# Performance work log

Hardware: AMD Instinct MI355X
Metric: run time of the kernel (lower is better)

The kernel has to match this reference:

```python
import jax, jax.numpy as jnp
import numpy as np

N = 100000
E = 1600000
F_IN = 32
H = 64
O = 64
L = 4
EPS = 1e-5


def setup_inputs() -> dict:
    key = jax.random.key(0)
    ks = jax.random.split(key, 16)
    x = jax.random.normal(ks[0], (N, F_IN), dtype=jnp.float32)
    edge_index = jax.random.randint(ks[1], (2, E), 0, N, dtype=jnp.int64)

    def xavier(k, shape):
        fan_in, fan_out = shape[-2], shape[-1]
        lim = (6.0 / (fan_in + fan_out)) ** 0.5
        return jax.random.uniform(k, shape, jnp.float32, -lim, lim)

    return {
        "x": x,
        "edge_index": edge_index,
        "W_embed": xavier(ks[2], (F_IN, H)),
        "b_embed": jnp.zeros((H,), jnp.float32),
        "conv_W": xavier(ks[3], (L, H, H)),
        "conv_b": jnp.zeros((L, H), jnp.float32),
        "bn_gamma": jnp.ones((L, H), jnp.float32),
        "bn_beta": jnp.zeros((L, H), jnp.float32),
        "W_out": xavier(ks[4], (H, O)),
        "b_out": jnp.zeros((O,), jnp.float32),
    }


def reference(x, edge_index, W_embed, b_embed, conv_W, conv_b, bn_gamma, bn_beta, W_out, b_out):
    src, dst = edge_index[0], edge_index[1]
    # GCN symmetric normalization with self-loops: deg counts incoming edges + 1
    deg = jax.ops.segment_sum(jnp.ones((E,), x.dtype), dst, num_segments=N) + 1.0
    dinv = deg ** -0.5                      # [N]
    norm_e = dinv[src] * dinv[dst]          # [E]
    self_norm = dinv * dinv                 # [N]  (self-loop weight)

    h = x @ W_embed + b_embed               # node embedding [N, H]

    for i in range(L):
        xw = h @ conv_W[i]                  # linear transform first (PyG GCNConv)
        msg = xw[src] * norm_e[:, None]     # gather + edge scaling [E, H]
        agg = jax.ops.segment_sum(msg, dst, num_segments=N)
        h = agg + xw * self_norm[:, None] + conv_b[i]
        # BatchNorm1d (training-mode batch stats, biased variance)
        mu = jnp.mean(h, axis=0)
        var = jnp.mean((h - mu) ** 2, axis=0)
        h = bn_gamma[i] * (h - mu) * jax.lax.rsqrt(var + EPS) + bn_beta[i]
        h = jax.nn.relu(h)
        # dropout is identity in inference

    pooled = jnp.mean(h, axis=0, keepdims=True)   # [1, H]
    return pooled @ W_out + b_out                 # [1, O]
```

## Files before the change

### kernel.cpp

```cpp
#include <hip/hip_runtime.h>

#define N_NODES 100000
#define N_EDGES 1600000
#define F_IN    32
#define HD      64
#define EPS     1e-5f
#define SCAN_B  512
#define SCAN_G  ((N_NODES + SCAN_B - 1) / SCAN_B)
#define NSHADOW 64
#define NP      196
#define PWS     9
#define NB1     250
#define EPB     6400

typedef __attribute__((ext_vector_type(8))) short short8v;
typedef __attribute__((ext_vector_type(4))) float f32x4;
typedef __attribute__((ext_vector_type(2))) float f32x2;

__device__ __forceinline__ unsigned bf16r(float f) {
    unsigned u = __float_as_uint(f);
    return (u + 0x7fffu + ((u >> 16) & 1u)) >> 16;
}
__device__ __forceinline__ unsigned pack2(float lo, float hi) {
    return bf16r(lo) | (bf16r(hi) << 16);
}
__device__ __forceinline__ float unlo(unsigned u) { return __uint_as_float(u << 16); }
__device__ __forceinline__ float unhi(unsigned u) { return __uint_as_float(u & 0xffff0000u); }

__device__ __forceinline__ unsigned pack_fp8x4(float a, float b, float c, float d) {
    int v = __builtin_amdgcn_cvt_pk_fp8_f32(a, b, 0, false);
    v = __builtin_amdgcn_cvt_pk_fp8_f32(c, d, v, true);
    return (unsigned)v;
}

__global__ void k_detect(const int* __restrict__ ei, int* __restrict__ flag) {
    if (threadIdx.x == 0 && blockIdx.x == 0) {
        int all_zero = 1;
        for (int k = 0; k < 64; ++k)
            if (ei[2 * k + 1] != 0) { all_zero = 0; break; }
        *flag = all_zero;
    }
}

__device__ __forceinline__ int load_src(const int* ei, int e, int is64) {
    return is64 ? ei[2 * e] : ei[e];
}
__device__ __forceinline__ int load_dst(const int* ei, int e, int is64) {
    return is64 ? ei[2 * (N_EDGES + e)] : ei[N_EDGES + e];
}

__global__ void __launch_bounds__(256)
k_p1_hist(const int* __restrict__ ei, const int* __restrict__ flag, int* __restrict__ hcnt) {
    __shared__ int hist[NP];
    int t = threadIdx.x, b = blockIdx.x;
    if (t < NP) hist[t] = 0;
    __syncthreads();
    int is64 = *flag;
#pragma unroll 5
    for (int i = 0; i < 25; ++i) {
        int e = b * EPB + i * 256 + t;
        int d = load_dst(ei, e, is64);
        atomicAdd(&hist[d >> PWS], 1);
    }
    __syncthreads();
    if (t < NP) hcnt[t * NB1 + b] = hist[t];
}

__global__ void k_p2scan(const int* __restrict__ hcnt, int* __restrict__ off_bp,
                         int* __restrict__ ptotal) {
    __shared__ int ls[256];
    int t = threadIdx.x, p = blockIdx.x;
    int v = (t < NB1) ? hcnt[p * NB1 + t] : 0;
    ls[t] = v;
    __syncthreads();
    for (int off = 1; off < 256; off <<= 1) {
        int u = (t >= off) ? ls[t - off] : 0;
        __syncthreads();
        ls[t] += u;
        __syncthreads();
    }
    if (t < NB1) off_bp[p * NB1 + t] = ls[t] - v;
    if (t == 255) ptotal[p] = ls[255];
}

__global__ void k_p3scan(const int* __restrict__ ptotal, int* __restrict__ pbase) {
    __shared__ int ls[256];
    int t = threadIdx.x;
    int v = (t < NP) ? ptotal[t] : 0;
    ls[t] = v;
    __syncthreads();
    for (int off = 1; off < 256; off <<= 1) {
        int u = (t >= off) ? ls[t - off] : 0;
        __syncthreads();
        ls[t] += u;
        __syncthreads();
    }
    if (t < NP) pbase[t] = ls[t] - v;
}

__global__ void __launch_bounds__(256)
k_p2_scatter(const int* __restrict__ ei, const int* __restrict__ flag,
             const int* __restrict__ off_bp, const int* __restrict__ pbase,
             uint2* __restrict__ part_buf) {
    __shared__ int cursor[NP];
    int t = threadIdx.x, b = blockIdx.x;
    if (t < NP) cursor[t] = pbase[t] + off_bp[t * NB1 + b];
    __syncthreads();
    int is64 = *flag;
#pragma unroll 5
    for (int i = 0; i < 25; ++i) {
        int e = b * EPB + i * 256 + t;
        int s = load_src(ei, e, is64);
        int d = load_dst(ei, e, is64);
        int slot = atomicAdd(&cursor[d >> PWS], 1);
        part_buf[slot] = make_uint2((unsigned)s, (unsigned)d);
    }
}

__global__ void __launch_bounds__(256)
k_p3a_deg(const uint2* __restrict__ part_buf, const int* __restrict__ pbase,
          const int* __restrict__ ptotal, int* __restrict__ deg,
          float* __restrict__ dinv) {
    __shared__ int hist[512];
    int t = threadIdx.x, p = blockIdx.x;
    hist[t] = 0; hist[t + 256] = 0;
    __syncthreads();
    int beg = pbase[p], cnt = ptotal[p];
    for (int r = t; r < cnt; r += 256)
        atomicAdd(&hist[part_buf[beg + r].y & 511], 1);
    __syncthreads();
    int n0 = (p << PWS) + t;
    if (n0 < N_NODES) {
        deg[n0] = hist[t];
        dinv[n0] = rsqrtf((float)hist[t] + 1.0f);
    }
    if (n0 + 256 < N_NODES) {
        deg[n0 + 256] = hist[t + 256];
        dinv[n0 + 256] = rsqrtf((float)hist[t + 256] + 1.0f);
    }
}

__global__ void __launch_bounds__(256)
k_p3b_csr(const uint2* __restrict__ part_buf, const int* __restrict__ pbase,
          const int* __restrict__ ptotal, const int* __restrict__ row_start,
          int* __restrict__ csr_src) {
    __shared__ int cur[512];
    int t = threadIdx.x, p = blockIdx.x;
    int n0 = (p << PWS) + t;
    cur[t]       = (n0 < N_NODES)       ? row_start[n0]       : 0;
    cur[t + 256] = (n0 + 256 < N_NODES) ? row_start[n0 + 256] : 0;
    __syncthreads();
    int beg = pbase[p], cnt = ptotal[p];
    for (int r = t; r < cnt; r += 256) {
        uint2 rec = part_buf[beg + r];
        int slot = atomicAdd(&cur[rec.y & 511], 1);
        csr_src[slot] = (int)rec.x;
    }
}

__global__ void k_scan1(const int* __restrict__ deg, int* __restrict__ bsum) {
    int t = threadIdx.x;
    int i = blockIdx.x * SCAN_B + t;
    __shared__ int ls[SCAN_B];
    ls[t] = (i < N_NODES) ? deg[i] : 0;
    __syncthreads();
    for (int off = SCAN_B / 2; off > 0; off >>= 1) {
        if (t < off) ls[t] += ls[t + off];
        __syncthreads();
    }
    if (t == 0) bsum[blockIdx.x] = ls[0];
}

__global__ void k_scan2(const int* __restrict__ bsum, int* __restrict__ boff,
                        int* __restrict__ row_start_last) {
    __shared__ int ls[256];
    int t = threadIdx.x;
    ls[t] = (t < SCAN_G) ? bsum[t] : 0;
    __syncthreads();
    for (int off = 1; off < 256; off <<= 1) {
        int u = (t >= off) ? ls[t - off] : 0;
        __syncthreads();
        ls[t] += u;
        __syncthreads();
    }
    boff[t] = (t == 0) ? 0 : ls[t - 1];
    if (t == 255) *row_start_last = ls[255];
}

__global__ void k_scan3(const int* __restrict__ deg, const int* __restrict__ boff,
                        int* __restrict__ row_start) {
    int t = threadIdx.x;
    int i = blockIdx.x * SCAN_B + t;
    int v = (i < N_NODES) ? deg[i] : 0;
    __shared__ int ls[SCAN_B];
    ls[t] = v;
    __syncthreads();
    for (int off = 1; off < SCAN_B; off <<= 1) {
        int u = (t >= off) ? ls[t - off] : 0;
        __syncthreads();
        ls[t] += u;
        __syncthreads();
    }
    if (i < N_NODES) row_start[i] = boff[blockIdx.x] + ls[t] - v;
}

__global__ void k_embed(const float* __restrict__ x, const float* __restrict__ W,
                        const float* __restrict__ b, unsigned* __restrict__ hb) {
    __shared__ float Ws[F_IN * HD];
    __shared__ float xs[4 * F_IN];
    int t = threadIdx.x;
    for (int i = t; i < F_IN * HD; i += 256) Ws[i] = W[i];
    if (t < 4 * F_IN) {
        int r = t >> 5, c = t & 31;
        int node = blockIdx.x * 4 + r;
        xs[t] = (node < N_NODES) ? x[node * F_IN + c] : 0.f;
    }
    __syncthreads();
    int r = t >> 6, j = t & 63;
    int node = blockIdx.x * 4 + r;
    float acc = b[j];
#pragma unroll
    for (int k = 0; k < F_IN; ++k)
        acc = fmaf(xs[r * F_IN + k], Ws[k * HD + j], acc);
    float other = __shfl_xor(acc, 1);
    if (node < N_NODES && (j & 1) == 0)
        hb[node * 32 + (j >> 1)] = pack2(acc, other);
}

__global__ void __launch_bounds__(256)
k_gemm_mfma(const unsigned* __restrict__ Ab, const float* __restrict__ W,
            const float* __restrict__ coef, const float* __restrict__ dinv,
            unsigned* __restrict__ Cf8) {
    __shared__ short Wt[64 * 72];
    __shared__ float Cs[4][16 * 66];
    int t = threadIdx.x;

    for (int i = t; i < HD * HD; i += 256) {
        int k = i >> 6, j = i & 63;
        Wt[j * 72 + k] = (short)bf16r(W[i]);
    }
    __syncthreads();

    int wid = t >> 6, lane = t & 63;
    int rlane = lane & 15, kb = lane >> 4;
    int base = blockIdx.x * 64 + wid * 16;
    int arow = base + rlane;
    if (arow > N_NODES - 1) arow = N_NODES - 1;
    bool has_coef = (coef != nullptr);

    short8v afrag[2];
#pragma unroll
    for (int h = 0; h < 2; ++h) {
        uint4 p = *reinterpret_cast<const uint4*>(Ab + arow * 32 + h * 16 + kb * 4);
        union { uint4 u; short8v s; } cv;
        if (has_coef) {
            int k0 = h * 32 + kb * 8;
            float v0 = unlo(p.x), v1 = unhi(p.x), v2 = unlo(p.y), v3 = unhi(p.y);
            float v4 = unlo(p.z), v5 = unhi(p.z), v6 = unlo(p.w), v7 = unhi(p.w);
            v0 = fmaxf(fmaf(coef[k0 + 0], v0, coef[64 + k0 + 0]), 0.f);
            v1 = fmaxf(fmaf(coef[k0 + 1], v1, coef[64 + k0 + 1]), 0.f);
            v2 = fmaxf(fmaf(coef[k0 + 2], v2, coef[64 + k0 + 2]), 0.f);
            v3 = fmaxf(fmaf(coef[k0 + 3], v3, coef[64 + k0 + 3]), 0.f);
            v4 = fmaxf(fmaf(coef[k0 + 4], v4, coef[64 + k0 + 4]), 0.f);
            v5 = fmaxf(fmaf(coef[k0 + 5], v5, coef[64 + k0 + 5]), 0.f);
            v6 = fmaxf(fmaf(coef[k0 + 6], v6, coef[64 + k0 + 6]), 0.f);
            v7 = fmaxf(fmaf(coef[k0 + 7], v7, coef[64 + k0 + 7]), 0.f);
            cv.u.x = pack2(v0, v1); cv.u.y = pack2(v2, v3);
            cv.u.z = pack2(v4, v5); cv.u.w = pack2(v6, v7);
        } else {
            cv.u = p;
        }
        afrag[h] = cv.s;
    }

    f32x4 acc[4];
#pragma unroll
    for (int nt = 0; nt < 4; ++nt) acc[nt] = (f32x4){0.f, 0.f, 0.f, 0.f};

#pragma unroll
    for (int nt = 0; nt < 4; ++nt) {
        int col = nt * 16 + rlane;
#pragma unroll
        for (int h = 0; h < 2; ++h) {
            short8v b = *reinterpret_cast<const short8v*>(&Wt[col * 72 + h * 32 + kb * 8]);
            acc[nt] = __builtin_amdgcn_mfma_f32_16x16x32_bf16(afrag[h], b, acc[nt], 0, 0, 0);
        }
    }

    float dv[4];
#pragma unroll
    for (int r = 0; r < 4; ++r) {
        int g = base + kb * 4 + r;
        dv[r] = dinv[g > N_NODES - 1 ? N_NODES - 1 : g];
    }
#pragma unroll
    for (int nt = 0; nt < 4; ++nt) {
        int col = nt * 16 + rlane;
#pragma unroll
        for (int r = 0; r < 4; ++r)
            Cs[wid][(kb * 4 + r) * 66 + col] = acc[nt][r] * dv[r];
    }
    __syncthreads();

#pragma unroll
    for (int u = 0; u < 4; ++u) {
        int o = u * 64 + lane;
        int row = o >> 4, q = o & 15;
        int node = blockIdx.x * 64 + wid * 16 + row;
        if (node < N_NODES) {
            const float* cp = &Cs[wid][row * 66 + q * 4];
            Cf8[node * 16 + q] = pack_fp8x4(cp[0], cp[1], cp[2], cp[3]);
        }
    }
}

__global__ void __launch_bounds__(256)
k_gather_stats(const unsigned* __restrict__ xwf8, const int* __restrict__ row_start,
               const int* __restrict__ csr_src, const float* __restrict__ dinv,
               const float* __restrict__ cb, uint2* __restrict__ hb2,
               float* __restrict__ stats_sh) {
    int t = threadIdx.x;
    int q = t & 15;
    int r = t >> 4;
    float cb0 = cb[q * 4 + 0], cb1 = cb[q * 4 + 1];
    float cb2 = cb[q * 4 + 2], cb3 = cb[q * 4 + 3];
    float4 st_s = {0.f, 0.f, 0.f, 0.f}, st_q = {0.f, 0.f, 0.f, 0.f};

#pragma unroll
    for (int i = 0; i < 4; ++i) {
        int n = blockIdx.x * 64 + r * 4 + i;
        bool valid = (n < N_NODES);
        int beg = 0, end = 0;
        if (valid) { beg = row_start[n]; end = row_start[n + 1]; }
        float4 a0 = {0.f,0.f,0.f,0.f}, a1 = {0.f,0.f,0.f,0.f};
        float4 a2 = {0.f,0.f,0.f,0.f}, a3 = {0.f,0.f,0.f,0.f};
        if (valid) {
            unsigned p = xwf8[n * 16 + q];
            f32x2 lo = __builtin_amdgcn_cvt_pk_f32_fp8((int)p, false);
            f32x2 hi = __builtin_amdgcn_cvt_pk_f32_fp8((int)p, true);
            a0.x = lo[0]; a0.y = lo[1]; a0.z = hi[0]; a0.w = hi[1];
        }
        int e = beg;
        for (; e + 3 < end; e += 4) {
            int s0 = csr_src[e],     s1 = csr_src[e + 1];
            int s2 = csr_src[e + 2], s3 = csr_src[e + 3];
            unsigned p0 = xwf8[s0 * 16 + q], p1 = xwf8[s1 * 16 + q];
            unsigned p2 = xwf8[s2 * 16 + q], p3 = xwf8[s3 * 16 + q];
            f32x2 l0 = __builtin_amdgcn_cvt_pk_f32_fp8((int)p0, false);
            f32x2 h0 = __builtin_amdgcn_cvt_pk_f32_fp8((int)p0, true);
            f32x2 l1 = __builtin_amdgcn_cvt_pk_f32_fp8((int)p1, false);
            f32x2 h1 = __builtin_amdgcn_cvt_pk_f32_fp8((int)p1, true);
            f32x2 l2 = __builtin_amdgcn_cvt_pk_f32_fp8((int)p2, false);
            f32x2 h2 = __builtin_amdgcn_cvt_pk_f32_fp8((int)p2, true);
            f32x2 l3 = __builtin_amdgcn_cvt_pk_f32_fp8((int)p3, false);
            f32x2 h3 = __builtin_amdgcn_cvt_pk_f32_fp8((int)p3, true);
            a0.x += l0[0]; a0.y += l0[1]; a0.z += h0[0]; a0.w += h0[1];
            a1.x += l1[0]; a1.y += l1[1]; a1.z += h1[0]; a1.w += h1[1];
            a2.x += l2[0]; a2.y += l2[1]; a2.z += h2[0]; a2.w += h2[1];
            a3.x += l3[0]; a3.y += l3[1]; a3.z += h3[0]; a3.w += h3[1];
        }
        for (; e < end; ++e) {
            int s0 = csr_src[e];
            unsigned p0 = xwf8[s0 * 16 + q];
            f32x2 l0 = __builtin_amdgcn_cvt_pk_f32_fp8((int)p0, false);
            f32x2 h0 = __builtin_amdgcn_cvt_pk_f32_fp8((int)p0, true);
            a0.x += l0[0]; a0.y += l0[1]; a0.z += h0[0]; a0.w += h0[1];
        }
        float dn = valid ? dinv[n] : 0.f;
        float4 h;
        h.x = fmaf(a0.x + a1.x + a2.x + a3.x, dn, cb0);
        h.y = fmaf(a0.y + a1.y + a2.y + a3.y, dn, cb1);
        h.z = fmaf(a0.z + a1.z + a2.z + a3.z, dn, cb2);
        h.w = fmaf(a0.w + a1.w + a2.w + a3.w, dn, cb3);
        if (valid) {
            uint2 o;
            o.x = pack2(h.x, h.y);
            o.y = pack2(h.z, h.w);
            hb2[n * 16 + q] = o;
            st_s.x += h.x; st_s.y += h.y; st_s.z += h.z; st_s.w += h.w;
            st_q.x = fmaf(h.x, h.x, st_q.x); st_q.y = fmaf(h.y, h.y, st_q.y);
            st_q.z = fmaf(h.z, h.z, st_q.z); st_q.w = fmaf(h.w, h.w, st_q.w);
        }
    }

    __shared__ float4 ls_s[256], ls_q[256];
    ls_s[t] = st_s; ls_q[t] = st_q;
    __syncthreads();
    if (t < 16) {
        float4 ss = ls_s[t], qq = ls_q[t];
        for (int rr = 1; rr < 16; ++rr) {
            float4 u = ls_s[rr * 16 + t], v = ls_q[rr * 16 + t];
            ss.x += u.x; ss.y += u.y; ss.z += u.z; ss.w += u.w;
            qq.x += v.x; qq.y += v.y; qq.z += v.z; qq.w += v.w;
        }
        float* sh = stats_sh + (blockIdx.x & (NSHADOW - 1)) * 128;
        atomicAdd(&sh[4 * t + 0], ss.x);
        atomicAdd(&sh[4 * t + 1], ss.y);
        atomicAdd(&sh[4 * t + 2], ss.z);
        atomicAdd(&sh[4 * t + 3], ss.w);
        atomicAdd(&sh[64 + 4 * t + 0], qq.x);
        atomicAdd(&sh[64 + 4 * t + 1], qq.y);
        atomicAdd(&sh[64 + 4 * t + 2], qq.z);
        atomicAdd(&sh[64 + 4 * t + 3], qq.w);
    }
}

__global__ void k_bn_coef(const float* __restrict__ stats_sh, const float* __restrict__ gamma,
                          const float* __restrict__ beta, float* __restrict__ coef) {
    int j = threadIdx.x;
    float s = 0.f, s2 = 0.f;
    for (int c = 0; c < NSHADOW; ++c) {
        s  += stats_sh[c * 128 + j];
        s2 += stats_sh[c * 128 + 64 + j];
    }
    float mu  = s * (1.0f / N_NODES);
    float var = s2 * (1.0f / N_NODES) - mu * mu;
    float rs  = rsqrtf(var + EPS);
    float a   = gamma[j] * rs;
    coef[j]      = a;
    coef[64 + j] = fmaf(-a, mu, beta[j]);
}

__global__ void k_pool(const unsigned* __restrict__ hb, const float* __restrict__ coef,
                       float* __restrict__ pooled) {
    int t = threadIdx.x;
    int j = t & 63, rg = t >> 6;
    float a = coef[j], c = coef[64 + j];
    float s = 0.f;
    for (int n = blockIdx.x * 4 + rg; n < N_NODES; n += gridDim.x * 4) {
        unsigned p = hb[n * 32 + (j >> 1)];
        float v = (j & 1) ? unhi(p) : unlo(p);
        s += fmaxf(fmaf(a, v, c), 0.f);
    }
    __shared__ float ls[256];
    ls[t] = s;
    __syncthreads();
    if (t < 64)
        atomicAdd(&pooled[j], ls[t] + ls[t + 64] + ls[t + 128] + ls[t + 192]);
}

__global__ void k_out(const float* __restrict__ pooled, const float* __restrict__ Wout,
                      const float* __restrict__ bout, float* __restrict__ out) {
    int o = threadIdx.x;
    float acc = bout[o];
#pragma unroll
    for (int k = 0; k < HD; ++k)
        acc = fmaf(pooled[k] * (1.0f / N_NODES), Wout[k * HD + o], acc);
    out[o] = acc;
}

extern "C" void kernel_launch(void* const* d_in, const int* in_sizes, int n_in,
                              void* d_out, int out_size, void* d_ws, size_t ws_size,
                              hipStream_t stream) {
    const float* x        = (const float*)d_in[0];
    const int*   ei       = (const int*)  d_in[1];
    const float* W_embed  = (const float*)d_in[2];
    const float* b_embed  = (const float*)d_in[3];
    const float* conv_W   = (const float*)d_in[4];
    const float* conv_b   = (const float*)d_in[5];
    const float* bn_gamma = (const float*)d_in[6];
    const float* bn_beta  = (const float*)d_in[7];
    const float* W_out    = (const float*)d_in[8];
    const float* b_out    = (const float*)d_in[9];
    float* out = (float*)d_out;

    float* ws = (float*)d_ws;
    int*   deg       = (int*)ws;
    float* dinv      = ws + N_NODES;
    int*   row_start = (int*)(ws + 2 * N_NODES);
    float* small     = ws + 3 * N_NODES + 8;
    int*   bsum      = (int*)small;
    int*   boff      = (int*)(small + 256);
    float* stats_sh  = small + 512;
    float* pooled    = small + 8704;
    float* coef      = small + 8768;
    int*   flag      = (int*)(small + 9280);
    int*   csr_src   = (int*)(small + 9344);
    int*   hcnt      = (int*)(small + 9344 + N_EDGES);
    int*   off_bp    = hcnt + NP * NB1;
    int*   ptotal    = off_bp + NP * NB1;
    int*   pbase     = ptotal + 256;
    uint2* part_buf  = (uint2*)(pbase + 256);
    float* bufA      = (float*)(part_buf + N_EDGES);
    float* bufB      = bufA + N_NODES * 32;

    k_detect<<<1, 64, 0, stream>>>(ei, flag);
    k_p1_hist<<<NB1, 256, 0, stream>>>(ei, flag, hcnt);
    k_p2scan<<<NP, 256, 0, stream>>>(hcnt, off_bp, ptotal);
    k_p3scan<<<1, 256, 0, stream>>>(ptotal, pbase);
    k_p2_scatter<<<NB1, 256, 0, stream>>>(ei, flag, off_bp, pbase, part_buf);
    k_p3a_deg<<<NP, 256, 0, stream>>>(part_buf, pbase, ptotal, deg, dinv);
    k_scan1<<<SCAN_G, SCAN_B, 0, stream>>>(deg, bsum);
    k_scan2<<<1, 256, 0, stream>>>(bsum, boff, ((int*)(ws + 2 * N_NODES)) + N_NODES);
    k_scan3<<<SCAN_G, SCAN_B, 0, stream>>>(deg, boff, row_start);
    k_embed<<<(N_NODES + 3) / 4, 256, 0, stream>>>(x, W_embed, b_embed, (unsigned*)bufA);
    k_p3b_csr<<<NP, 256, 0, stream>>>(part_buf, pbase, ptotal, row_start, csr_src);

    for (int l = 0; l < 4; ++l) {
        k_gemm_mfma<<<(N_NODES + 63) / 64, 256, 0, stream>>>(
            (const unsigned*)bufA, conv_W + l * HD * HD,
            l ? coef + (l - 1) * 128 : nullptr, dinv, (unsigned*)bufB);
        hipMemsetAsync(stats_sh, 0, NSHADOW * 128 * sizeof(float), stream);
        k_gather_stats<<<(N_NODES + 63) / 64, 256, 0, stream>>>(
            (const unsigned*)bufB, row_start, csr_src, dinv, conv_b + l * HD,
            (uint2*)bufA, stats_sh);
        k_bn_coef<<<1, 64, 0, stream>>>(stats_sh, bn_gamma + l * HD, bn_beta + l * HD,
                                        coef + l * 128);
    }

    hipMemsetAsync(pooled, 0, 64 * sizeof(float), stream);
    k_pool<<<1024, 256, 0, stream>>>((const unsigned*)bufA, coef + 3 * 128, pooled);
    k_out<<<1, 64, 0, stream>>>(pooled, W_out, b_out, out);
}
```

Before: 348.2 us.

## Split gather into two feature-half planes and fuse CSR build with scan

The GEMM now writes its fp8 output as two separate 32-feature planes, and the gather kernel runs twice per layer, once per plane. Each pass touches a 3.2MB working set, which makes random row gathers more likely to hit in cache, at the cost of reading the CSR indices twice. The degree count, prefix scan and CSR fill are merged into one per-partition kernel with a local block scan, removing four launches and the deg array. Stats buffers for all layers are cleared by one memset up front instead of one per layer.

```diff
diff --git a/kernel.cpp b/kernel.cpp
--- a/kernel.cpp
+++ b/kernel.cpp
@@ -5,13 +5,12 @@
 #define F_IN    32
 #define HD      64
 #define EPS     1e-5f
-#define SCAN_B  512
-#define SCAN_G  ((N_NODES + SCAN_B - 1) / SCAN_B)
 #define NSHADOW 64
 #define NP      196
 #define PWS     9
 #define NB1     250
 #define EPB     6400
+#define NPLANE  (N_NODES * 8)
 
 typedef __attribute__((ext_vector_type(8))) short short8v;
 typedef __attribute__((ext_vector_type(4))) float f32x4;
@@ -118,10 +117,12 @@
 }
 
 __global__ void __launch_bounds__(256)
-k_p3a_deg(const uint2* __restrict__ part_buf, const int* __restrict__ pbase,
-          const int* __restrict__ ptotal, int* __restrict__ deg,
-          float* __restrict__ dinv) {
+k_p3_build(const uint2* __restrict__ part_buf, const int* __restrict__ pbase,
+           const int* __restrict__ ptotal, int* __restrict__ row_start,
+           float* __restrict__ dinv, int* __restrict__ csr_src) {
     __shared__ int hist[512];
+    __shared__ int s2[256];
+    __shared__ int cur[512];
     int t = threadIdx.x, p = blockIdx.x;
     hist[t] = 0; hist[t + 256] = 0;
     __syncthreads();
@@ -129,79 +130,28 @@
     for (int r = t; r < cnt; r += 256)
         atomicAdd(&hist[part_buf[beg + r].y & 511], 1);
     __syncthreads();
-    int n0 = (p << PWS) + t;
-    if (n0 < N_NODES) {
-        deg[n0] = hist[t];
-        dinv[n0] = rsqrtf((float)hist[t] + 1.0f);
-    }
-    if (n0 + 256 < N_NODES) {
-        deg[n0 + 256] = hist[t + 256];
-        dinv[n0 + 256] = rsqrtf((float)hist[t + 256] + 1.0f);
-    }
-}
-
-__global__ void __launch_bounds__(256)
-k_p3b_csr(const uint2* __restrict__ part_buf, const int* __restrict__ pbase,
-          const int* __restrict__ ptotal, const int* __restrict__ row_start,
-          int* __restrict__ csr_src) {
-    __shared__ int cur[512];
-    int t = threadIdx.x, p = blockIdx.x;
-    int n0 = (p << PWS) + t;
-    cur[t]       = (n0 < N_NODES)       ? row_start[n0]       : 0;
-    cur[t + 256] = (n0 + 256 < N_NODES) ? row_start[n0 + 256] : 0;
-    __syncthreads();
-    int beg = pbase[p], cnt = ptotal[p];
+    int d0 = hist[2 * t], d1 = hist[2 * t + 1];
+    s2[t] = d0 + d1;
+    __syncthreads();
+    for (int off = 1; off < 256; off <<= 1) {
+        int u = (t >= off) ? s2[t - off] : 0;
+        __syncthreads();
+        s2[t] += u;
+        __syncthreads();
+    }
+    int ex = (t == 0) ? 0 : s2[t - 1];
+    int rs0 = beg + ex, rs1 = beg + ex + d0;
+    int n0 = (p << PWS) + 2 * t;
+    if (n0 < N_NODES)     { row_start[n0]     = rs0; dinv[n0]     = rsqrtf((float)d0 + 1.f); }
+    if (n0 + 1 < N_NODES) { row_start[n0 + 1] = rs1; dinv[n0 + 1] = rsqrtf((float)d1 + 1.f); }
+    cur[2 * t] = rs0; cur[2 * t + 1] = rs1;
+    if (p == NP - 1 && t == 0) row_start[N_NODES] = N_EDGES;
+    __syncthreads();
     for (int r = t; r < cnt; r += 256) {
         uint2 rec = part_buf[beg + r];
         int slot = atomicAdd(&cur[rec.y & 511], 1);
         csr_src[slot] = (int)rec.x;
     }
-}
-
-__global__ void k_scan1(const int* __restrict__ deg, int* __restrict__ bsum) {
-    int t = threadIdx.x;
-    int i = blockIdx.x * SCAN_B + t;
-    __shared__ int ls[SCAN_B];
-    ls[t] = (i < N_NODES) ? deg[i] : 0;
-    __syncthreads();
-    for (int off = SCAN_B / 2; off > 0; off >>= 1) {
-        if (t < off) ls[t] += ls[t + off];
-        __syncthreads();
-    }
-    if (t == 0) bsum[blockIdx.x] = ls[0];
-}
-
-__global__ void k_scan2(const int* __restrict__ bsum, int* __restrict__ boff,
-                        int* __restrict__ row_start_last) {
-    __shared__ int ls[256];
-    int t = threadIdx.x;
-    ls[t] = (t < SCAN_G) ? bsum[t] : 0;
-    __syncthreads();
-    for (int off = 1; off < 256; off <<= 1) {
-        int u = (t >= off) ? ls[t - off] : 0;
-        __syncthreads();
-        ls[t] += u;
-        __syncthreads();
-    }
-    boff[t] = (t == 0) ? 0 : ls[t - 1];
-    if (t == 255) *row_start_last = ls[255];
-}
-
-__global__ void k_scan3(const int* __restrict__ deg, const int* __restrict__ boff,
-                        int* __restrict__ row_start) {
-    int t = threadIdx.x;
-    int i = blockIdx.x * SCAN_B + t;
-    int v = (i < N_NODES) ? deg[i] : 0;
-    __shared__ int ls[SCAN_B];
-    ls[t] = v;
-    __syncthreads();
-    for (int off = 1; off < SCAN_B; off <<= 1) {
-        int u = (t >= off) ? ls[t - off] : 0;
-        __syncthreads();
-        ls[t] += u;
-        __syncthreads();
-    }
-    if (i < N_NODES) row_start[i] = boff[blockIdx.x] + ls[t] - v;
 }
 
 __global__ void k_embed(const float* __restrict__ x, const float* __restrict__ W,
@@ -309,33 +259,35 @@
         int node = blockIdx.x * 64 + wid * 16 + row;
         if (node < N_NODES) {
             const float* cp = &Cs[wid][row * 66 + q * 4];
-            Cf8[node * 16 + q] = pack_fp8x4(cp[0], cp[1], cp[2], cp[3]);
+            unsigned val = pack_fp8x4(cp[0], cp[1], cp[2], cp[3]);
+            if (q < 8) Cf8[node * 8 + q] = val;
+            else       Cf8[NPLANE + node * 8 + (q - 8)] = val;
         }
     }
 }
 
 __global__ void __launch_bounds__(256)
-k_gather_stats(const unsigned* __restrict__ xwf8, const int* __restrict__ row_start,
+k_gather_stats(const unsigned* __restrict__ plane, const int* __restrict__ row_start,
                const int* __restrict__ csr_src, const float* __restrict__ dinv,
-               const float* __restrict__ cb, uint2* __restrict__ hb2,
-               float* __restrict__ stats_sh) {
+               const float* __restrict__ cb ,
+               uint2* __restrict__ hb2, float* __restrict__ stats_sh, int qoff) {
     int t = threadIdx.x;
-    int q = t & 15;
-    int r = t >> 4;
+    int q = t & 7;
+    int r = t >> 3;
     float cb0 = cb[q * 4 + 0], cb1 = cb[q * 4 + 1];
     float cb2 = cb[q * 4 + 2], cb3 = cb[q * 4 + 3];
     float4 st_s = {0.f, 0.f, 0.f, 0.f}, st_q = {0.f, 0.f, 0.f, 0.f};
 
 #pragma unroll
     for (int i = 0; i < 4; ++i) {
-        int n = blockIdx.x * 64 + r * 4 + i;
+        int n = blockIdx.x * 128 + r * 4 + i;
         bool valid = (n < N_NODES);
         int beg = 0, end = 0;
         if (valid) { beg = row_start[n]; end = row_start[n + 1]; }
         float4 a0 = {0.f,0.f,0.f,0.f}, a1 = {0.f,0.f,0.f,0.f};
         float4 a2 = {0.f,0.f,0.f,0.f}, a3 = {0.f,0.f,0.f,0.f};
         if (valid) {
-            unsigned p = xwf8[n * 16 + q];
+            unsigned p = plane[n * 8 + q];
             f32x2 lo = __builtin_amdgcn_cvt_pk_f32_fp8((int)p, false);
             f32x2 hi = __builtin_amdgcn_cvt_pk_f32_fp8((int)p, true);
             a0.x = lo[0]; a0.y = lo[1]; a0.z = hi[0]; a0.w = hi[1];
@@ -344,8 +296,8 @@
         for (; e + 3 < end; e += 4) {
             int s0 = csr_src[e],     s1 = csr_src[e + 1];
             int s2 = csr_src[e + 2], s3 = csr_src[e + 3];
-            unsigned p0 = xwf8[s0 * 16 + q], p1 = xwf8[s1 * 16 + q];
-            unsigned p2 = xwf8[s2 * 16 + q], p3 = xwf8[s3 * 16 + q];
+            unsigned p0 = plane[s0 * 8 + q], p1 = plane[s1 * 8 + q];
+            unsigned p2 = plane[s2 * 8 + q], p3 = plane[s3 * 8 + q];
             f32x2 l0 = __builtin_amdgcn_cvt_pk_f32_fp8((int)p0, false);
             f32x2 h0 = __builtin_amdgcn_cvt_pk_f32_fp8((int)p0, true);
             f32x2 l1 = __builtin_amdgcn_cvt_pk_f32_fp8((int)p1, false);
@@ -361,7 +313,7 @@
         }
         for (; e < end; ++e) {
             int s0 = csr_src[e];
-            unsigned p0 = xwf8[s0 * 16 + q];
+            unsigned p0 = plane[s0 * 8 + q];
             f32x2 l0 = __builtin_amdgcn_cvt_pk_f32_fp8((int)p0, false);
             f32x2 h0 = __builtin_amdgcn_cvt_pk_f32_fp8((int)p0, true);
             a0.x += l0[0]; a0.y += l0[1]; a0.z += h0[0]; a0.w += h0[1];
@@ -376,7 +328,7 @@
             uint2 o;
             o.x = pack2(h.x, h.y);
             o.y = pack2(h.z, h.w);
-            hb2[n * 16 + q] = o;
+            hb2[n * 16 + qoff + q] = o;
             st_s.x += h.x; st_s.y += h.y; st_s.z += h.z; st_s.w += h.w;
             st_q.x = fmaf(h.x, h.x, st_q.x); st_q.y = fmaf(h.y, h.y, st_q.y);
             st_q.z = fmaf(h.z, h.z, st_q.z); st_q.w = fmaf(h.w, h.w, st_q.w);
@@ -386,22 +338,23 @@
     __shared__ float4 ls_s[256], ls_q[256];
     ls_s[t] = st_s; ls_q[t] = st_q;
     __syncthreads();
-    if (t < 16) {
+    if (t < 8) {
         float4 ss = ls_s[t], qq = ls_q[t];
-        for (int rr = 1; rr < 16; ++rr) {
-            float4 u = ls_s[rr * 16 + t], v = ls_q[rr * 16 + t];
+        for (int rr = 1; rr < 32; ++rr) {
+            float4 u = ls_s[rr * 8 + t], v = ls_q[rr * 8 + t];
             ss.x += u.x; ss.y += u.y; ss.z += u.z; ss.w += u.w;
             qq.x += v.x; qq.y += v.y; qq.z += v.z; qq.w += v.w;
         }
         float* sh = stats_sh + (blockIdx.x & (NSHADOW - 1)) * 128;
-        atomicAdd(&sh[4 * t + 0], ss.x);
-        atomicAdd(&sh[4 * t + 1], ss.y);
-        atomicAdd(&sh[4 * t + 2], ss.z);
-        atomicAdd(&sh[4 * t + 3], ss.w);
-        atomicAdd(&sh[64 + 4 * t + 0], qq.x);
-        atomicAdd(&sh[64 + 4 * t + 1], qq.y);
-        atomicAdd(&sh[64 + 4 * t + 2], qq.z);
-        atomicAdd(&sh[64 + 4 * t + 3], qq.w);
+        int j0 = qoff * 4 + 4 * t;
+        atomicAdd(&sh[j0 + 0], ss.x);
+        atomicAdd(&sh[j0 + 1], ss.y);
+        atomicAdd(&sh[j0 + 2], ss.z);
+        atomicAdd(&sh[j0 + 3], ss.w);
+        atomicAdd(&sh[64 + j0 + 0], qq.x);
+        atomicAdd(&sh[64 + j0 + 1], qq.y);
+        atomicAdd(&sh[64 + j0 + 2], qq.z);
+        atomicAdd(&sh[64 + j0 + 3], qq.w);
     }
 }
 
@@ -465,18 +418,15 @@
     float* out = (float*)d_out;
 
     float* ws = (float*)d_ws;
-    int*   deg       = (int*)ws;
-    float* dinv      = ws + N_NODES;
-    int*   row_start = (int*)(ws + 2 * N_NODES);
-    float* small     = ws + 3 * N_NODES + 8;
-    int*   bsum      = (int*)small;
-    int*   boff      = (int*)(small + 256);
-    float* stats_sh  = small + 512;
-    float* pooled    = small + 8704;
-    float* coef      = small + 8768;
-    int*   flag      = (int*)(small + 9280);
-    int*   csr_src   = (int*)(small + 9344);
-    int*   hcnt      = (int*)(small + 9344 + N_EDGES);
+    float* dinv      = ws;
+    int*   row_start = (int*)(ws + N_NODES);
+    float* small     = ws + 2 * N_NODES + 8;
+    float* stats_sh  = small;
+    float* pooled    = small + 32768;
+    float* coef      = small + 32832;
+    int*   flag      = (int*)(small + 33344);
+    int*   csr_src   = (int*)(small + 33408);
+    int*   hcnt      = (int*)(small + 33408 + N_EDGES);
     int*   off_bp    = hcnt + NP * NB1;
     int*   ptotal    = off_bp + NP * NB1;
     int*   pbase     = ptotal + 256;
@@ -489,22 +439,22 @@
     k_p2scan<<<NP, 256, 0, stream>>>(hcnt, off_bp, ptotal);
     k_p3scan<<<1, 256, 0, stream>>>(ptotal, pbase);
     k_p2_scatter<<<NB1, 256, 0, stream>>>(ei, flag, off_bp, pbase, part_buf);
-    k_p3a_deg<<<NP, 256, 0, stream>>>(part_buf, pbase, ptotal, deg, dinv);
-    k_scan1<<<SCAN_G, SCAN_B, 0, stream>>>(deg, bsum);
-    k_scan2<<<1, 256, 0, stream>>>(bsum, boff, ((int*)(ws + 2 * N_NODES)) + N_NODES);
-    k_scan3<<<SCAN_G, SCAN_B, 0, stream>>>(deg, boff, row_start);
+    k_p3_build<<<NP, 256, 0, stream>>>(part_buf, pbase, ptotal, row_start, dinv, csr_src);
     k_embed<<<(N_NODES + 3) / 4, 256, 0, stream>>>(x, W_embed, b_embed, (unsigned*)bufA);
-    k_p3b_csr<<<NP, 256, 0, stream>>>(part_buf, pbase, ptotal, row_start, csr_src);
+    hipMemsetAsync(stats_sh, 0, 4 * NSHADOW * 128 * sizeof(float), stream);
 
     for (int l = 0; l < 4; ++l) {
+        float* st = stats_sh + l * NSHADOW * 128;
         k_gemm_mfma<<<(N_NODES + 63) / 64, 256, 0, stream>>>(
             (const unsigned*)bufA, conv_W + l * HD * HD,
             l ? coef + (l - 1) * 128 : nullptr, dinv, (unsigned*)bufB);
-        hipMemsetAsync(stats_sh, 0, NSHADOW * 128 * sizeof(float), stream);
-        k_gather_stats<<<(N_NODES + 63) / 64, 256, 0, stream>>>(
-            (const unsigned*)bufB, row_start, csr_src, dinv, conv_b + l * HD,
-            (uint2*)bufA, stats_sh);
-        k_bn_coef<<<1, 64, 0, stream>>>(stats_sh, bn_gamma + l * HD, bn_beta + l * HD,
+        k_gather_stats<<<(N_NODES + 127) / 128, 256, 0, stream>>>(
+            (const unsigned*)bufB, row_start, csr_src, dinv,
+            conv_b + l * HD, (uint2*)bufA, st, 0);
+        k_gather_stats<<<(N_NODES + 127) / 128, 256, 0, stream>>>(
+            (const unsigned*)bufB + NPLANE, row_start, csr_src, dinv,
+            conv_b + l * HD + 32, (uint2*)bufA, st, 8);
+        k_bn_coef<<<1, 64, 0, stream>>>(st, bn_gamma + l * HD, bn_beta + l * HD,
                                         coef + l * 128);
     }
 
```

New measurement: 427.7 us. +22.8%, slower.
